# Kernel optimization log

Hardware: AMD Instinct MI355X
Metric: run time of the kernel (lower is better)

The kernel has to match this reference:

```python
import jax, jax.numpy as jnp
import numpy as np

B, T, C, H = 4, 2048, 1024, 16
HD = C // H  # head_dim = 64


def setup_inputs() -> dict:
    key = jax.random.key(0)
    k1, k2, k3 = jax.random.split(key, 3)
    x = jax.random.normal(k1, (B, T, C), dtype=jnp.float32)
    W_qkv = jax.random.normal(k2, (C, 3 * C), dtype=jnp.float32) * (1.0 / np.sqrt(C))
    W_out = jax.random.normal(k3, (C, C), dtype=jnp.float32) * (1.0 / np.sqrt(C))
    return {"x": x, "W_qkv": W_qkv, "W_out": W_out}


def reference(x, W_qkv, W_out):
    Bx, Tx, Cx = x.shape
    qkv = jnp.einsum('btc,cd->btd', x, W_qkv)  # [B,T,3C]
    q, k, v = jnp.split(qkv, 3, axis=-1)
    # [B,T,C] -> [B,H,T,HD]
    q = q.reshape(Bx, Tx, H, HD).transpose(0, 2, 1, 3)
    k = k.reshape(Bx, Tx, H, HD).transpose(0, 2, 1, 3)
    v = v.reshape(Bx, Tx, H, HD).transpose(0, 2, 1, 3)
    scale = 1.0 / jnp.sqrt(jnp.asarray(HD, dtype=x.dtype))
    attn = jnp.einsum('bhqd,bhkd->bhqk', q, k) * scale  # [B,H,T,T]
    causal = jnp.tril(jnp.ones((Tx, Tx), dtype=bool))
    attn = jnp.where(causal, attn, jnp.asarray(-1e9, dtype=attn.dtype))
    attn = jax.nn.softmax(attn, axis=-1)
    out = jnp.einsum('bhqk,bhkd->bhqd', attn, v)  # [B,H,T,HD]
    out = out.transpose(0, 2, 1, 3).reshape(Bx, Tx, Cx)
    return jnp.einsum('btc,cd->btd', out, W_out)
```

## Files before the change

kernel.cpp:

```cpp
#include <hip/hip_runtime.h>
#include <hip/hip_bf16.h>
#include <cstdint>


typedef __attribute__((ext_vector_type(8))) short bf16x8;
typedef __attribute__((ext_vector_type(4))) float f32x4;
typedef __attribute__((ext_vector_type(4))) uint32_t u32x4;

#define MFMA_BF16(a, b, c) __builtin_amdgcn_mfma_f32_16x16x32_bf16((a), (b), (c), 0, 0, 0)

__device__ __forceinline__ ushort f2bf(float f) {
  union { float f; uint32_t u; } x;
  x.f = f;
  uint32_t u = x.u;
  return (ushort)((u + 0x7FFFu + ((u >> 16) & 1u)) >> 16);
}

__device__ __forceinline__ uint32_t cvt_pk_bf16(float lo, float hi) {
  uint32_t r;
  asm("v_cvt_pk_bf16_f32 %0, %1, %2" : "=v"(r) : "v"(lo), "v"(hi));
  return r;
}

__device__ __forceinline__ void gload16(const ushort* g, ushort* l) {
  __builtin_amdgcn_global_load_lds(
      (const __attribute__((address_space(1))) void*)g,
      (__attribute__((address_space(3))) void*)l, 16, 0, 0);
}

__global__ __launch_bounds__(256) void convert_f32_bf16(
    const float* __restrict__ in, ushort* __restrict__ out, int n4) {
  int i = blockIdx.x * 256 + threadIdx.x;
  if (i < n4) {
    float4 v = ((const float4*)in)[i];
    ushort4 o;
    o.x = f2bf(v.x); o.y = f2bf(v.y); o.z = f2bf(v.z); o.w = f2bf(v.w);
    ((ushort4*)out)[i] = o;
  }
}

__global__ __launch_bounds__(256) void transpose_w(
    const float* __restrict__ W, ushort* __restrict__ Wt, int K, int N) {
  __shared__ float tile[32][33];
  const int n0 = blockIdx.x * 32, k0 = blockIdx.y * 32;
  const int tx = threadIdx.x & 31, ty = threadIdx.x >> 5;
#pragma unroll
  for (int i = 0; i < 4; ++i)
    tile[ty + i * 8][tx] = W[(size_t)(k0 + ty + i * 8) * N + n0 + tx];
  __syncthreads();
#pragma unroll
  for (int i = 0; i < 4; ++i)
    Wt[(size_t)(n0 + ty + i * 8) * K + k0 + tx] = f2bf(tile[tx][ty + i * 8]);
}

template <int MODE>
__global__ __launch_bounds__(256)
__attribute__((amdgpu_waves_per_eu(3, 3)))
void gemm_bf16_kernel(
    const ushort* __restrict__ A, const ushort* __restrict__ Bt,
    float* __restrict__ C,
    ushort* __restrict__ qb, ushort* __restrict__ kb, ushort* __restrict__ vb,
    int M, int N, int K) {
  __shared__ ushort As[3][128 * 32];
  __shared__ ushort Bs[3][128 * 32];
  const int tid = threadIdx.x;
  const int lane = tid & 63;
  const int w = tid >> 6;
  const int wr = w >> 1, wc = w & 1;
  const int l15 = lane & 15, lhi = lane >> 4;

  const int ncolt = N >> 7;
  const int rpx = (M >> 7) >> 3;
  const int b = blockIdx.x;
  const int xcd = b & 7;
  const int loc = b >> 3;
  const int rowg = loc / ncolt;
  const int colt = loc - rowg * ncolt;
  const int row0 = (xcd * rpx + rowg) * 128;
  const int col0 = colt * 128;

  const int cr = lane >> 2;
  const int sl = lane & 3;
  const int gofs = (sl ^ ((cr >> 1) & 3)) << 3;
  const ushort* gA = A  + (size_t)(row0 + w * 32 + cr) * K + gofs;
  const ushort* gB = Bt + (size_t)(col0 + w * 32 + cr) * K + gofs;
  const int lbase = (w * 32) * 32;

  f32x4 acc[4][4] = {};

#define G_STAGE(BUF, T)                                                      \
  {                                                                          \
    gload16(gA + (size_t)(T) * 32, &As[BUF][lbase]);                         \
    gload16(gA + (size_t)16 * K + (size_t)(T) * 32, &As[BUF][lbase + 512]);  \
    gload16(gB + (size_t)(T) * 32, &Bs[BUF][lbase]);                         \
    gload16(gB + (size_t)16 * K + (size_t)(T) * 32, &Bs[BUF][lbase + 512]);  \
  }

  const int nk = K >> 5;
  G_STAGE(0, 0)
  G_STAGE(1, 1)

  for (int t = 0; t < nk; ++t) {
    const int cur = t % 3;
    if (t + 1 < nk) {
      asm volatile("s_waitcnt vmcnt(4)" ::: "memory");
    } else {
      asm volatile("s_waitcnt vmcnt(0)" ::: "memory");
    }
    __builtin_amdgcn_s_barrier();

    bf16x8 af[4], bfr[4];
#pragma unroll
    for (int m = 0; m < 4; ++m) {
      const int row = wr * 64 + m * 16 + l15;
      af[m] = *(const bf16x8*)&As[cur][row * 32 + ((lhi ^ ((row >> 1) & 3)) << 3)];
    }
#pragma unroll
    for (int n = 0; n < 4; ++n) {
      const int row = wc * 64 + n * 16 + l15;
      bfr[n] = *(const bf16x8*)&Bs[cur][row * 32 + ((lhi ^ ((row >> 1) & 3)) << 3)];
    }

    if (t + 2 < nk) {
      const int nb = (t + 2) % 3;
      G_STAGE(nb, t + 2)
    }

    __builtin_amdgcn_s_setprio(1);
#pragma unroll
    for (int m = 0; m < 4; ++m)
#pragma unroll
      for (int n = 0; n < 4; ++n)
        acc[m][n] = MFMA_BF16(af[m], bfr[n], acc[m][n]);
    __builtin_amdgcn_s_setprio(0);
  }
#undef G_STAGE

  if (MODE == 1) {
#pragma unroll
    for (int m = 0; m < 4; ++m) {
      const int r0 = row0 + wr * 64 + m * 16 + lhi * 4;
#pragma unroll
      for (int n = 0; n < 4; ++n) {
        const int c = col0 + wc * 64 + n * 16 + l15;
#pragma unroll
        for (int j = 0; j < 4; ++j)
          C[(size_t)(r0 + j) * N + c] = acc[m][n][j];
      }
    }
  } else {
    const float QSCALE = 0.18033688011112042f;
#pragma unroll
    for (int m = 0; m < 4; ++m) {
      const int r0 = row0 + wr * 64 + m * 16 + lhi * 4;
      const int b_ = r0 >> 11;
      const int t0 = r0 & 2047;
#pragma unroll
      for (int n = 0; n < 4; ++n) {
        const int c = col0 + wc * 64 + n * 16 + l15;
        const int seg = c >> 10;
        const int cc = c & 1023;
        const int h = cc >> 6, d = cc & 63;
        const size_t bhi = (size_t)(b_ * 16 + h);
        if (seg == 0) {
#pragma unroll
          for (int j = 0; j < 4; ++j)
            qb[(bhi * 2048 + t0 + j) * 64 + d] = f2bf(acc[m][n][j] * QSCALE);
        } else if (seg == 1) {
#pragma unroll
          for (int j = 0; j < 4; ++j)
            kb[(bhi * 2048 + t0 + j) * 64 + d] = f2bf(acc[m][n][j]);
        } else {
          const int pos = (t0 & ~31) + ((t0 & 12) << 1) + ((t0 >> 4) & 1) * 4;
          ushort4 pk;
          pk.x = f2bf(acc[m][n][0]);
          pk.y = f2bf(acc[m][n][1]);
          pk.z = f2bf(acc[m][n][2]);
          pk.w = f2bf(acc[m][n][3]);
          *(ushort4*)(vb + (bhi * 64 + d) * 2048 + pos) = pk;
        }
      }
    }
  }
}

#define QK_TILE(SV, KT)                                                      \
  {                                                                          \
    const int krow = (KT) * 16 + l15;                                        \
    const int sw = krow & 7;                                                 \
    bf16x8 kf0 = *(const bf16x8*)&Ks[cur][krow * 64 + ((lhi ^ sw) * 8)];     \
    bf16x8 kf1 = *(const bf16x8*)&Ks[cur][krow * 64 + (((4 + lhi) ^ sw) * 8)];\
    f32x4 acc_ = {};                                                         \
    acc_ = MFMA_BF16(kf0, qf0, acc_);                                        \
    acc_ = MFMA_BF16(kf1, qf1, acc_);                                        \
    SV = acc_;                                                               \
  }

#define MASK_TILE(SV, KT)                                                    \
  {                                                                          \
    if (key0 + (KT) * 16 + lhi * 4 + 0 > qrow) SV[0] = -INFINITY;            \
    if (key0 + (KT) * 16 + lhi * 4 + 1 > qrow) SV[1] = -INFINITY;            \
    if (key0 + (KT) * 16 + lhi * 4 + 2 > qrow) SV[2] = -INFINITY;            \
    if (key0 + (KT) * 16 + lhi * 4 + 3 > qrow) SV[3] = -INFINITY;            \
  }

#define SM_TILE(SV, W0, W1)                                                  \
  {                                                                          \
    float p0 = exp2f(SV[0] - m_state);                                       \
    float p1 = exp2f(SV[1] - m_state);                                       \
    float p2 = exp2f(SV[2] - m_state);                                       \
    float p3 = exp2f(SV[3] - m_state);                                       \
    lloc += (p0 + p1) + (p2 + p3);                                           \
    W0 = cvt_pk_bf16(p0, p1);                                                \
    W1 = cvt_pk_bf16(p2, p3);                                                \
  }

#define PV_TILE(ON, N)                                                       \
  {                                                                          \
    const int vrow = (N) * 16 + l15;                                         \
    const int sw = vrow & 7;                                                 \
    bf16x8 vf0 = *(const bf16x8*)&Vs[cur][vrow * 64 + ((lhi ^ sw) * 8)];     \
    bf16x8 vf1 = *(const bf16x8*)&Vs[cur][vrow * 64 + (((4 + lhi) ^ sw) * 8)];\
    ON = MFMA_BF16(pf0, vf0, ON);                                            \
    ON = MFMA_BF16(pf1, vf1, ON);                                            \
  }

__global__ __launch_bounds__(256)
__attribute__((amdgpu_waves_per_eu(4, 4)))
void attn_kernel(
    const ushort* __restrict__ Qb, const ushort* __restrict__ Kb,
    const ushort* __restrict__ Vt, ushort* __restrict__ Ab) {
  const int bid = blockIdx.x;
  const int qt = 31 - (bid >> 6);
  const int bh = bid & 63;
  const int tid = threadIdx.x;
  const int lane = tid & 63;
  const int w = tid >> 6;
  const int l15 = lane & 15, lhi = lane >> 4;
  const int qloc = qt * 64 + w * 16;

  __shared__ ushort Ks[2][64 * 64];
  __shared__ ushort Vs[2][64 * 64];

  const size_t qkbase = (size_t)bh * (2048 * 64);
  const size_t vtb = (size_t)bh * (64 * 2048);

  const int srow = w * 16 + (lane >> 3);
  const int sd0 = lane & 7;
  const int slot = (sd0 ^ (srow & 7)) * 8;

  const ushort* kp0 = Kb + qkbase + (size_t)srow * 64 + sd0 * 8;
  const ushort* kp1 = kp0 + 8 * 64;
  const ushort* vp0 = Vt + vtb + (size_t)srow * 2048 + sd0 * 8;
  const ushort* vp1 = vp0 + 8 * 2048;

  bf16x8 qf0 = *(const bf16x8*)(Qb + qkbase + (size_t)(qloc + l15) * 64 + lhi * 8);
  bf16x8 qf1 = *(const bf16x8*)(Qb + qkbase + (size_t)(qloc + l15) * 64 + 32 + lhi * 8);

  uint4 kr0 = *(const uint4*)kp0;
  uint4 kr1 = *(const uint4*)kp1;
  uint4 vr0 = *(const uint4*)vp0;
  uint4 vr1 = *(const uint4*)vp1;
  *(uint4*)&Ks[0][srow * 64 + slot] = kr0;
  *(uint4*)&Ks[0][(srow + 8) * 64 + slot] = kr1;
  *(uint4*)&Vs[0][srow * 64 + slot] = vr0;
  *(uint4*)&Vs[0][(srow + 8) * 64 + slot] = vr1;
  __syncthreads();

  float m_state = -INFINITY, l_state = 0.f;
  f32x4 o0 = {}, o1 = {}, o2 = {}, o3 = {};
  const int qrow = qloc + l15;
  int cur = 0;

  for (int kbt = 0; kbt <= qt; ++kbt) {
    const int key0 = kbt * 64;
    const bool last = (kbt == qt);

    if (!last) {
      const size_t koff = (size_t)(kbt + 1) * 64 * 64;
      kr0 = *(const uint4*)(kp0 + koff);
      kr1 = *(const uint4*)(kp1 + koff);
      vr0 = *(const uint4*)(vp0 + (kbt + 1) * 64);
      vr1 = *(const uint4*)(vp1 + (kbt + 1) * 64);
    }

    f32x4 s0, s1, s2, s3;
    __builtin_amdgcn_s_setprio(1);
    QK_TILE(s0, 0)
    QK_TILE(s1, 1)
    QK_TILE(s2, 2)
    QK_TILE(s3, 3)
    __builtin_amdgcn_s_setprio(0);

    if (last) {
      MASK_TILE(s0, 0)
      MASK_TILE(s1, 1)
      MASK_TILE(s2, 2)
      MASK_TILE(s3, 3)
    }

    float t0 = fmaxf(fmaxf(s0[0], s0[1]), fmaxf(s0[2], s0[3]));
    float t1 = fmaxf(fmaxf(s1[0], s1[1]), fmaxf(s1[2], s1[3]));
    float t2 = fmaxf(fmaxf(s2[0], s2[1]), fmaxf(s2[2], s2[3]));
    float t3 = fmaxf(fmaxf(s3[0], s3[1]), fmaxf(s3[2], s3[3]));
    float tmax = fmaxf(fmaxf(t0, t1), fmaxf(t2, t3));
    tmax = fmaxf(tmax, __shfl_xor(tmax, 16));
    tmax = fmaxf(tmax, __shfl_xor(tmax, 32));

    if (!__all(tmax <= m_state + 8.0f)) {
      const float mnew = fmaxf(m_state, tmax);
      const float alpha = exp2f(m_state - mnew);
      const float a0 = __shfl(alpha, lhi * 4 + 0);
      const float a1 = __shfl(alpha, lhi * 4 + 1);
      const float a2 = __shfl(alpha, lhi * 4 + 2);
      const float a3 = __shfl(alpha, lhi * 4 + 3);
      o0[0] *= a0; o0[1] *= a1; o0[2] *= a2; o0[3] *= a3;
      o1[0] *= a0; o1[1] *= a1; o1[2] *= a2; o1[3] *= a3;
      o2[0] *= a0; o2[1] *= a1; o2[2] *= a2; o2[3] *= a3;
      o3[0] *= a0; o3[1] *= a1; o3[2] *= a2; o3[3] *= a3;
      l_state *= alpha;
      m_state = mnew;
    }

    float lloc = 0.f;
    uint32_t w0, w1, w2, w3, w4, w5, w6, w7;
    SM_TILE(s0, w0, w1)
    SM_TILE(s1, w2, w3)
    SM_TILE(s2, w4, w5)
    SM_TILE(s3, w6, w7)
    lloc += __shfl_xor(lloc, 16);
    lloc += __shfl_xor(lloc, 32);
    l_state += lloc;

    u32x4 pw0 = {w0, w1, w2, w3};
    u32x4 pw1 = {w4, w5, w6, w7};
    bf16x8 pf0 = __builtin_bit_cast(bf16x8, pw0);
    bf16x8 pf1 = __builtin_bit_cast(bf16x8, pw1);

    __builtin_amdgcn_s_setprio(1);
    PV_TILE(o0, 0)
    PV_TILE(o1, 1)
    PV_TILE(o2, 2)
    PV_TILE(o3, 3)
    __builtin_amdgcn_s_setprio(0);

    if (!last) {
      const int nxt = cur ^ 1;
      *(uint4*)&Ks[nxt][srow * 64 + slot] = kr0;
      *(uint4*)&Ks[nxt][(srow + 8) * 64 + slot] = kr1;
      *(uint4*)&Vs[nxt][srow * 64 + slot] = vr0;
      *(uint4*)&Vs[nxt][(srow + 8) * 64 + slot] = vr1;
      cur = nxt;
      __syncthreads();
    }
  }

  const int b_ = bh >> 4, h_ = bh & 15;
#pragma unroll
  for (int j = 0; j < 4; ++j) {
    const float linv = 1.0f / __shfl(l_state, lhi * 4 + j);
    const int t = qloc + lhi * 4 + j;
    const size_t ro = ((size_t)b_ * 2048 + t) * 1024 + h_ * 64;
    Ab[ro + 0 * 16 + l15] = f2bf(o0[j] * linv);
    Ab[ro + 1 * 16 + l15] = f2bf(o1[j] * linv);
    Ab[ro + 2 * 16 + l15] = f2bf(o2[j] * linv);
    Ab[ro + 3 * 16 + l15] = f2bf(o3[j] * linv);
  }
}

extern "C" void kernel_launch(void* const* d_in, const int* in_sizes, int n_in,
                              void* d_out, int out_size, void* d_ws, size_t ws_size,
                              hipStream_t stream) {
  const float* x = (const float*)d_in[0];
  const float* Wqkv = (const float*)d_in[1];
  const float* Wout = (const float*)d_in[2];
  float* out = (float*)d_out;

  ushort* xb    = (ushort*)d_ws;
  ushort* wqkvT = xb + (size_t)8192 * 1024;
  ushort* woutT = wqkvT + (size_t)3072 * 1024;
  ushort* qb    = woutT + (size_t)1024 * 1024;
  ushort* kbuf  = qb + (size_t)64 * 2048 * 64;
  ushort* vbuf  = kbuf + (size_t)64 * 2048 * 64;
  ushort* ab    = vbuf + (size_t)64 * 2048 * 64;

  convert_f32_bf16<<<8192, 256, 0, stream>>>(x, xb, 8192 * 1024 / 4);
  transpose_w<<<dim3(96, 32), 256, 0, stream>>>(Wqkv, wqkvT, 1024, 3072);
  transpose_w<<<dim3(32, 32), 256, 0, stream>>>(Wout, woutT, 1024, 1024);
  gemm_bf16_kernel<0><<<1536, 256, 0, stream>>>(
      xb, wqkvT, nullptr, qb, kbuf, vbuf, 8192, 3072, 1024);
  attn_kernel<<<2048, 256, 0, stream>>>(qb, kbuf, vbuf, ab);
  gemm_bf16_kernel<1><<<512, 256, 0, stream>>>(
      ab, woutT, out, nullptr, nullptr, nullptr, 8192, 1024, 1024);
}
```

Before: 178.8 us.

## Replace QKV projection GEMM with 256x256-tile, 8-wave double-buffered kernel

Adds a new QKV GEMM kernel using 256x256 output tiles, 512 threads, K-step 64, double-buffered LDS with XOR swizzle, and an interleaved LDS-load/MFMA schedule with barriers and setprio. It also maps blocks to XCDs so that row groups stay local. The larger tile raises arithmetic intensity per byte loaded and cuts the block count from 1536 to 384. The risk is lower occupancy (2 waves per EU, large LDS), register pressure from 32 accumulators, and a tail effect with 384 blocks over 256 CUs. The epilogue scatter to the q/k/v layouts is kept as before, including the pre-scaled Q and the permuted V.

```diff
diff --git a/kernel.cpp b/kernel.cpp
--- a/kernel.cpp
+++ b/kernel.cpp
@@ -51,6 +51,160 @@
 #pragma unroll
   for (int i = 0; i < 4; ++i)
     Wt[(size_t)(n0 + ty + i * 8) * K + k0 + tx] = f2bf(tile[tx][ty + i * 8]);
+}
+
+
+#define LD_AF(MH)                                                            \
+  {                                                                          \
+    _Pragma("unroll")                                                        \
+    for (int m = 0; m < 4; ++m) {                                            \
+      const int row = wr * 128 + (MH) * 64 + m * 16 + l15;                   \
+      _Pragma("unroll")                                                      \
+      for (int kk = 0; kk < 2; ++kk)                                         \
+        af[m][kk] = *(const bf16x8*)&as[row * 64 +                           \
+                     (((kk * 4 + lhi) ^ (row & 7)) << 3)];                   \
+    }                                                                        \
+  }
+
+#define LD_BF(DST, NH)                                                       \
+  {                                                                          \
+    _Pragma("unroll")                                                        \
+    for (int n = 0; n < 2; ++n) {                                            \
+      const int row = wc * 64 + (NH) * 32 + n * 16 + l15;                    \
+      _Pragma("unroll")                                                      \
+      for (int kk = 0; kk < 2; ++kk)                                         \
+        DST[n][kk] = *(const bf16x8*)&bs[row * 64 +                          \
+                     (((kk * 4 + lhi) ^ (row & 7)) << 3)];                   \
+    }                                                                        \
+  }
+
+#define MFMA16(MH, NH, BF)                                                   \
+  {                                                                          \
+    __builtin_amdgcn_s_setprio(1);                                           \
+    _Pragma("unroll")                                                        \
+    for (int m = 0; m < 4; ++m)                                              \
+      _Pragma("unroll")                                                      \
+      for (int n = 0; n < 2; ++n)                                            \
+        _Pragma("unroll")                                                    \
+        for (int kk = 0; kk < 2; ++kk)                                       \
+          acc[(MH) * 4 + m][(NH) * 2 + n] = MFMA_BF16(                       \
+              af[m][kk], BF[n][kk], acc[(MH) * 4 + m][(NH) * 2 + n]);        \
+    __builtin_amdgcn_s_setprio(0);                                           \
+  }
+
+__global__ __launch_bounds__(512)
+__attribute__((amdgpu_waves_per_eu(2, 2)))
+void gemm256_qkv(
+    const ushort* __restrict__ A, const ushort* __restrict__ Bt,
+    ushort* __restrict__ qb, ushort* __restrict__ kb, ushort* __restrict__ vb,
+    int M, int N, int K) {
+  __shared__ ushort As[2][256 * 64];
+  __shared__ ushort Bs[2][256 * 64];
+  const int tid = threadIdx.x;
+  const int lane = tid & 63;
+  const int w = tid >> 6;
+  const int wr = w >> 2, wc = w & 3;
+  const int l15 = lane & 15, lhi = lane >> 4;
+
+  const int ncolt = N >> 8;
+  const int rpx = (M >> 8) >> 3;
+  const int b = blockIdx.x;
+  const int xcd = b & 7;
+  const int loc = b >> 3;
+  const int rowg = loc / ncolt;
+  const int colt = loc - rowg * ncolt;
+  const int row0 = (xcd * rpx + rowg) * 256;
+  const int col0 = colt * 256;
+
+  const int cr = lane >> 3;
+  const int sl = lane & 7;
+  const int gofs = (sl ^ cr) << 3;
+  const ushort* gA = A  + (size_t)(row0 + w * 32 + cr) * K + gofs;
+  const ushort* gB = Bt + (size_t)(col0 + w * 32 + cr) * K + gofs;
+  const int lb = (w * 32) * 64;
+
+#define G_STAGE8(BUF, T)                                                     \
+  {                                                                          \
+    _Pragma("unroll")                                                        \
+    for (int c = 0; c < 4; ++c) {                                            \
+      gload16(gA + (size_t)(c * 8) * K + (size_t)(T) * 64,                   \
+              &As[BUF][lb + c * 512]);                                       \
+      gload16(gB + (size_t)(c * 8) * K + (size_t)(T) * 64,                   \
+              &Bs[BUF][lb + c * 512]);                                       \
+    }                                                                        \
+  }
+
+  f32x4 acc[8][4] = {};
+
+  const int nk = K >> 6;
+  G_STAGE8(0, 0)
+  asm volatile("s_waitcnt vmcnt(0)" ::: "memory");
+  __builtin_amdgcn_s_barrier();
+
+  for (int t = 0; t < nk; ++t) {
+    const int cur = t & 1;
+    const ushort* as = &As[cur][0];
+    const ushort* bs = &Bs[cur][0];
+    const bool pre = (t + 1 < nk);
+
+    bf16x8 af[4][2], bf0[2][2], bf1[2][2];
+
+    if (pre) G_STAGE8(cur ^ 1, t + 1)
+    LD_AF(0)
+    LD_BF(bf0, 0)
+    __builtin_amdgcn_s_barrier();
+    MFMA16(0, 0, bf0)
+    __builtin_amdgcn_s_barrier();
+
+    LD_BF(bf1, 1)
+    __builtin_amdgcn_s_barrier();
+    MFMA16(0, 1, bf1)
+    __builtin_amdgcn_s_barrier();
+
+    LD_AF(1)
+    __builtin_amdgcn_s_barrier();
+    MFMA16(1, 1, bf1)
+    __builtin_amdgcn_s_barrier();
+
+    __builtin_amdgcn_s_barrier();
+    MFMA16(1, 0, bf0)
+    if (pre) asm volatile("s_waitcnt vmcnt(0)" ::: "memory");
+    __builtin_amdgcn_s_barrier();
+  }
+#undef G_STAGE8
+
+  const float QSCALE = 0.18033688011112042f;
+#pragma unroll
+  for (int m = 0; m < 8; ++m) {
+    const int r0 = row0 + wr * 128 + m * 16 + lhi * 4;
+    const int b_ = r0 >> 11;
+    const int t0 = r0 & 2047;
+#pragma unroll
+    for (int n = 0; n < 4; ++n) {
+      const int c = col0 + wc * 64 + n * 16 + l15;
+      const int seg = c >> 10;
+      const int cc = c & 1023;
+      const int h = cc >> 6, d = cc & 63;
+      const size_t bhi = (size_t)(b_ * 16 + h);
+      if (seg == 0) {
+#pragma unroll
+        for (int j = 0; j < 4; ++j)
+          qb[(bhi * 2048 + t0 + j) * 64 + d] = f2bf(acc[m][n][j] * QSCALE);
+      } else if (seg == 1) {
+#pragma unroll
+        for (int j = 0; j < 4; ++j)
+          kb[(bhi * 2048 + t0 + j) * 64 + d] = f2bf(acc[m][n][j]);
+      } else {
+        const int pos = (t0 & ~31) + ((t0 & 12) << 1) + ((t0 >> 4) & 1) * 4;
+        ushort4 pk;
+        pk.x = f2bf(acc[m][n][0]);
+        pk.y = f2bf(acc[m][n][1]);
+        pk.z = f2bf(acc[m][n][2]);
+        pk.w = f2bf(acc[m][n][3]);
+        *(ushort4*)(vb + (bhi * 64 + d) * 2048 + pos) = pk;
+      }
+    }
+  }
 }
 
 template <int MODE>
@@ -387,8 +541,8 @@
   convert_f32_bf16<<<8192, 256, 0, stream>>>(x, xb, 8192 * 1024 / 4);
   transpose_w<<<dim3(96, 32), 256, 0, stream>>>(Wqkv, wqkvT, 1024, 3072);
   transpose_w<<<dim3(32, 32), 256, 0, stream>>>(Wout, woutT, 1024, 1024);
-  gemm_bf16_kernel<0><<<1536, 256, 0, stream>>>(
-      xb, wqkvT, nullptr, qb, kbuf, vbuf, 8192, 3072, 1024);
+  gemm256_qkv<<<384, 512, 0, stream>>>(
+      xb, wqkvT, qb, kbuf, vbuf, 8192, 3072, 1024);
   attn_kernel<<<2048, 256, 0, stream>>>(qb, kbuf, vbuf, ab);
   gemm_bf16_kernel<1><<<512, 256, 0, stream>>>(
       ab, woutT, out, nullptr, nullptr, nullptr, 8192, 1024, 1024);
```

New measurement: 193.9 us. +8.4%, slower.

## Split output projection into dedicated GEMM with BK=64 double-buffered tiles

Applied to the files above, without the earlier changes.

The templated GEMM is split in two: the QKV GEMM keeps its three-stage BK=32 pipeline, and a new output-projection kernel uses 64-wide K tiles with double buffering, an XOR swizzle, waves_per_eu set to 2, and a plain 2D grid with no XCD remapping. Larger K tiles halve the number of barrier and loop iterations for the 512-block output GEMM. In exchange each block uses more LDS, which lowers occupancy, and dropping the XCD-aware block ordering may hurt L2 locality.

```diff
diff --git a/kernel.cpp b/kernel.cpp
--- a/kernel.cpp
+++ b/kernel.cpp
@@ -53,12 +53,10 @@
     Wt[(size_t)(n0 + ty + i * 8) * K + k0 + tx] = f2bf(tile[tx][ty + i * 8]);
 }
 
-template <int MODE>
 __global__ __launch_bounds__(256)
 __attribute__((amdgpu_waves_per_eu(3, 3)))
-void gemm_bf16_kernel(
+void gemm_qkv(
     const ushort* __restrict__ A, const ushort* __restrict__ Bt,
-    float* __restrict__ C,
     ushort* __restrict__ qb, ushort* __restrict__ kb, ushort* __restrict__ vb,
     int M, int N, int K) {
   __shared__ ushort As[3][128 * 32];
@@ -136,50 +134,116 @@
   }
 #undef G_STAGE
 
-  if (MODE == 1) {
-#pragma unroll
-    for (int m = 0; m < 4; ++m) {
-      const int r0 = row0 + wr * 64 + m * 16 + lhi * 4;
+  const float QSCALE = 0.18033688011112042f;
+#pragma unroll
+  for (int m = 0; m < 4; ++m) {
+    const int r0 = row0 + wr * 64 + m * 16 + lhi * 4;
+    const int b_ = r0 >> 11;
+    const int t0 = r0 & 2047;
+#pragma unroll
+    for (int n = 0; n < 4; ++n) {
+      const int c = col0 + wc * 64 + n * 16 + l15;
+      const int seg = c >> 10;
+      const int cc = c & 1023;
+      const int h = cc >> 6, d = cc & 63;
+      const size_t bhi = (size_t)(b_ * 16 + h);
+      if (seg == 0) {
+#pragma unroll
+        for (int j = 0; j < 4; ++j)
+          qb[(bhi * 2048 + t0 + j) * 64 + d] = f2bf(acc[m][n][j] * QSCALE);
+      } else if (seg == 1) {
+#pragma unroll
+        for (int j = 0; j < 4; ++j)
+          kb[(bhi * 2048 + t0 + j) * 64 + d] = f2bf(acc[m][n][j]);
+      } else {
+        const int pos = (t0 & ~31) + ((t0 & 12) << 1) + ((t0 >> 4) & 1) * 4;
+        ushort4 pk;
+        pk.x = f2bf(acc[m][n][0]);
+        pk.y = f2bf(acc[m][n][1]);
+        pk.z = f2bf(acc[m][n][2]);
+        pk.w = f2bf(acc[m][n][3]);
+        *(ushort4*)(vb + (bhi * 64 + d) * 2048 + pos) = pk;
+      }
+    }
+  }
+}
+
+__global__ __launch_bounds__(256)
+__attribute__((amdgpu_waves_per_eu(2, 2)))
+void gemm_out(
+    const ushort* __restrict__ A, const ushort* __restrict__ Bt,
+    float* __restrict__ C, int M, int N, int K) {
+  __shared__ ushort As[2][128 * 64];
+  __shared__ ushort Bs[2][128 * 64];
+  const int tid = threadIdx.x;
+  const int lane = tid & 63;
+  const int w = tid >> 6;
+  const int wr = w >> 1, wc = w & 1;
+  const int l15 = lane & 15, lhi = lane >> 4;
+  const int row0 = blockIdx.x * 128, col0 = blockIdx.y * 128;
+
+  const int cr = lane >> 3;
+  const int sl = lane & 7;
+  const int gofs = (sl ^ cr) << 3;
+  const ushort* gA = A  + (size_t)(row0 + w * 32 + cr) * K + gofs;
+  const ushort* gB = Bt + (size_t)(col0 + w * 32 + cr) * K + gofs;
+  const int lbase = (w * 32) * 64;
+
+  f32x4 acc[4][4] = {};
+
+#define G_STAGE8(BUF, K0)                                                    \
+  {                                                                          \
+    _Pragma("unroll")                                                        \
+    for (int i = 0; i < 4; ++i) {                                            \
+      gload16(gA + (size_t)(i * 8) * K + (K0), &As[BUF][lbase + i * 512]);   \
+      gload16(gB + (size_t)(i * 8) * K + (K0), &Bs[BUF][lbase + i * 512]);   \
+    }                                                                        \
+  }
+
+  const int nk = K >> 6;
+  G_STAGE8(0, 0)
+  __syncthreads();
+
+  for (int t = 0; t < nk; ++t) {
+    const int cur = t & 1;
+    if (t + 1 < nk) G_STAGE8(cur ^ 1, (t + 1) << 6)
+
+#pragma unroll
+    for (int kh = 0; kh < 2; ++kh) {
+      bf16x8 af[4], bfr[4];
+#pragma unroll
+      for (int m = 0; m < 4; ++m) {
+        const int row = wr * 64 + m * 16 + l15;
+        const int s = kh * 4 + lhi;
+        af[m] = *(const bf16x8*)&As[cur][row * 64 + ((s ^ (row & 7)) << 3)];
+      }
 #pragma unroll
       for (int n = 0; n < 4; ++n) {
-        const int c = col0 + wc * 64 + n * 16 + l15;
-#pragma unroll
-        for (int j = 0; j < 4; ++j)
-          C[(size_t)(r0 + j) * N + c] = acc[m][n][j];
+        const int row = wc * 64 + n * 16 + l15;
+        const int s = kh * 4 + lhi;
+        bfr[n] = *(const bf16x8*)&Bs[cur][row * 64 + ((s ^ (row & 7)) << 3)];
       }
-    }
-  } else {
-    const float QSCALE = 0.18033688011112042f;
-#pragma unroll
-    for (int m = 0; m < 4; ++m) {
-      const int r0 = row0 + wr * 64 + m * 16 + lhi * 4;
-      const int b_ = r0 >> 11;
-      const int t0 = r0 & 2047;
-#pragma unroll
-      for (int n = 0; n < 4; ++n) {
-        const int c = col0 + wc * 64 + n * 16 + l15;
-        const int seg = c >> 10;
-        const int cc = c & 1023;
-        const int h = cc >> 6, d = cc & 63;
-        const size_t bhi = (size_t)(b_ * 16 + h);
-        if (seg == 0) {
-#pragma unroll
-          for (int j = 0; j < 4; ++j)
-            qb[(bhi * 2048 + t0 + j) * 64 + d] = f2bf(acc[m][n][j] * QSCALE);
-        } else if (seg == 1) {
-#pragma unroll
-          for (int j = 0; j < 4; ++j)
-            kb[(bhi * 2048 + t0 + j) * 64 + d] = f2bf(acc[m][n][j]);
-        } else {
-          const int pos = (t0 & ~31) + ((t0 & 12) << 1) + ((t0 >> 4) & 1) * 4;
-          ushort4 pk;
-          pk.x = f2bf(acc[m][n][0]);
-          pk.y = f2bf(acc[m][n][1]);
-          pk.z = f2bf(acc[m][n][2]);
-          pk.w = f2bf(acc[m][n][3]);
-          *(ushort4*)(vb + (bhi * 64 + d) * 2048 + pos) = pk;
-        }
-      }
+      __builtin_amdgcn_s_setprio(1);
+#pragma unroll
+      for (int m = 0; m < 4; ++m)
+#pragma unroll
+        for (int n = 0; n < 4; ++n)
+          acc[m][n] = MFMA_BF16(af[m], bfr[n], acc[m][n]);
+      __builtin_amdgcn_s_setprio(0);
+    }
+    __syncthreads();
+  }
+#undef G_STAGE8
+
+#pragma unroll
+  for (int m = 0; m < 4; ++m) {
+    const int r0 = row0 + wr * 64 + m * 16 + lhi * 4;
+#pragma unroll
+    for (int n = 0; n < 4; ++n) {
+      const int c = col0 + wc * 64 + n * 16 + l15;
+#pragma unroll
+      for (int j = 0; j < 4; ++j)
+        C[(size_t)(r0 + j) * N + c] = acc[m][n][j];
     }
   }
 }
@@ -387,9 +451,9 @@
   convert_f32_bf16<<<8192, 256, 0, stream>>>(x, xb, 8192 * 1024 / 4);
   transpose_w<<<dim3(96, 32), 256, 0, stream>>>(Wqkv, wqkvT, 1024, 3072);
   transpose_w<<<dim3(32, 32), 256, 0, stream>>>(Wout, woutT, 1024, 1024);
-  gemm_bf16_kernel<0><<<1536, 256, 0, stream>>>(
-      xb, wqkvT, nullptr, qb, kbuf, vbuf, 8192, 3072, 1024);
+  gemm_qkv<<<1536, 256, 0, stream>>>(
+      xb, wqkvT, qb, kbuf, vbuf, 8192, 3072, 1024);
   attn_kernel<<<2048, 256, 0, stream>>>(qb, kbuf, vbuf, ab);
-  gemm_bf16_kernel<1><<<512, 256, 0, stream>>>(
-      ab, woutT, out, nullptr, nullptr, nullptr, 8192, 1024, 1024);
-}
+  gemm_out<<<dim3(64, 8), 256, 0, stream>>>(
+      ab, woutT, out, 8192, 1024, 1024);
+}
```

Measured after the change: 178.1 us. About the same (-0.4%).
